# Kernel tuning notes

Measured on AMD Instinct MI355X. Metric: run time of the kernel, lower is better.

The kernel has to match this reference:

```python
import jax, jax.numpy as jnp
import numpy as np

COST_CLASS = 1.0
COST_BBOX = 5.0
COST_GIOU = 2.0
BS, NQ, NC, M = 16, 1000, 92, 1024


def box_cxcywh_to_xyxy(x):
    xc, yc, w, h = jnp.split(x, 4, axis=-1)
    return jnp.concatenate([xc - 0.5 * w, yc - 0.5 * h, xc + 0.5 * w, yc + 0.5 * h], axis=-1)


def generalized_box_iou(a, b):
    # a: [N,4] xyxy, b: [M,4] xyxy -> [N,M]
    area_a = (a[:, 2] - a[:, 0]) * (a[:, 3] - a[:, 1])
    area_b = (b[:, 2] - b[:, 0]) * (b[:, 3] - b[:, 1])
    lt = jnp.maximum(a[:, None, :2], b[None, :, :2])  # [N,M,2]
    rb = jnp.minimum(a[:, None, 2:], b[None, :, 2:])
    wh = jnp.clip(rb - lt, 0.0)
    inter = wh[..., 0] * wh[..., 1]
    union = area_a[:, None] + area_b[None, :] - inter
    iou = inter / union
    lt_e = jnp.minimum(a[:, None, :2], b[None, :, :2])
    rb_e = jnp.maximum(a[:, None, 2:], b[None, :, 2:])
    wh_e = jnp.clip(rb_e - lt_e, 0.0)
    area_e = wh_e[..., 0] * wh_e[..., 1]
    return iou - (area_e - union) / area_e


def setup_inputs() -> dict:
    key = jax.random.key(0)
    k1, k2, k3, k4 = jax.random.split(key, 4)
    return {
        'pred_logits': jax.random.normal(k1, (BS, NQ, NC), dtype=jnp.float32),
        'pred_boxes': jax.random.uniform(k2, (BS, NQ, 4), dtype=jnp.float32),
        'tgt_boxes': jax.random.uniform(k3, (M, 4), dtype=jnp.float32),
        'tgt_labels': jax.random.randint(k4, (M,), 0, NC),
    }


def reference(pred_logits, pred_boxes, tgt_boxes, tgt_labels):
    bs, nq, nc = pred_logits.shape
    out_prob = jax.nn.softmax(pred_logits.reshape(bs * nq, nc), axis=-1)
    out_bbox = pred_boxes.reshape(bs * nq, 4)
    tgt_ids = jnp.clip(tgt_labels, 0, nc - 1)
    # classification cost: -prob of target class, gathered per target -> [N, M]
    cost_class = -out_prob[:, tgt_ids]
    # L1 cdist on cxcywh boxes -> [N, M]
    cost_bbox = jnp.abs(out_bbox[:, None, :] - tgt_bbox_b(tgt_boxes)[None, :, :]).sum(-1)
    cost_giou = -generalized_box_iou(box_cxcywh_to_xyxy(out_bbox), box_cxcywh_to_xyxy(tgt_boxes))
    C = COST_BBOX * cost_bbox + COST_CLASS * cost_class + COST_GIOU * cost_giou
    return C.reshape(bs, nq, -1)


def tgt_bbox_b(tgt_boxes):
    return tgt_boxes
```

## Files before the change

kernel.cpp:

```cpp
#include <hip/hip_runtime.h>
#include <math.h>


#define NROWS 16000
#define NC 92
#define M_TGT 1024
#define TPB 256
#define ROWS 8
#define KPT 4

typedef float f32x4 __attribute__((ext_vector_type(4)));

__global__ __launch_bounds__(TPB, 6) void hungarian_cost_kernel(
    const float* __restrict__ logits,
    const float* __restrict__ pboxes,
    const float* __restrict__ tboxes,
    const int*   __restrict__ tlabels,
    float* __restrict__ out)
{
    const int n0 = blockIdx.x * ROWS;
    const int t = threadIdx.x;
    const int lane = t & 63;
    const int wid  = t >> 6;

    __shared__ float negp[ROWS][NC];

    #pragma unroll
    for (int j = 0; j < 2; ++j) {
        const int r = wid * 2 + j;
        const float* lg = logits + (size_t)(n0 + r) * NC;
        const float x0 = lg[lane];
        const bool  hi = (lane < NC - 64);
        const float x1 = hi ? lg[64 + lane] : -INFINITY;
        float mx = fmaxf(x0, x1);
        #pragma unroll
        for (int off = 32; off >= 1; off >>= 1)
            mx = fmaxf(mx, __shfl_xor(mx, off));
        const float e0 = __expf(x0 - mx);
        const float e1 = hi ? __expf(x1 - mx) : 0.0f;
        float s = e0 + e1;
        #pragma unroll
        for (int off = 32; off >= 1; off >>= 1)
            s += __shfl_xor(s, off);
        const float rs = __builtin_amdgcn_rcpf(s);
        negp[r][lane] = fmaf(-e0, rs, 2.0f);
        if (hi) negp[r][64 + lane] = fmaf(-e1, rs, 2.0f);
    }

    float tcx[KPT], tcy[KPT], twd[KPT], tht[KPT];
    float bx0[KPT], by0[KPT], bx1[KPT], by1[KPT], areab[KPT];
    const int4 lb4 = reinterpret_cast<const int4*>(tlabels)[t];
    int lbl[KPT] = {lb4.x, lb4.y, lb4.z, lb4.w};
    #pragma unroll
    for (int k = 0; k < KPT; ++k) {
        const float4 tb = reinterpret_cast<const float4*>(tboxes)[4 * t + k];
        tcx[k] = tb.x; tcy[k] = tb.y; twd[k] = tb.z; tht[k] = tb.w;
        bx0[k] = fmaf(-0.5f, tb.z, tb.x);  by0[k] = fmaf(-0.5f, tb.w, tb.y);
        bx1[k] = fmaf( 0.5f, tb.z, tb.x);  by1[k] = fmaf( 0.5f, tb.w, tb.y);
        areab[k] = tb.z * tb.w;
        lbl[k] = (lbl[k] < 0) ? 0 : (lbl[k] > NC - 1 ? NC - 1 : lbl[k]);
    }
    __syncthreads();

    float cls[KPT];
    #pragma unroll
    for (int k = 0; k < KPT; ++k) cls[k] = negp[0][lbl[k]];
    float4 pb = reinterpret_cast<const float4*>(pboxes)[n0];

    #pragma unroll
    for (int r = 0; r < ROWS; ++r) {
        float clsN[KPT];
        float4 pbN;
        if (r + 1 < ROWS) {
            #pragma unroll
            for (int k = 0; k < KPT; ++k) clsN[k] = negp[r + 1][lbl[k]];
            pbN = reinterpret_cast<const float4*>(pboxes)[n0 + r + 1];
        }

        const float ax0 = fmaf(-0.5f, pb.z, pb.x);
        const float ay0 = fmaf(-0.5f, pb.w, pb.y);
        const float ax1 = fmaf( 0.5f, pb.z, pb.x);
        const float ay1 = fmaf( 0.5f, pb.w, pb.y);
        const float area_a = pb.z * pb.w;

        float tmp[KPT];
        #pragma unroll
        for (int k = 0; k < KPT; ++k) {
            const float cb = fabsf(pb.x - tcx[k]) + fabsf(pb.y - tcy[k])
                           + fabsf(pb.z - twd[k]) + fabsf(pb.w - tht[k]);
            const float iwu = fminf(ax1, bx1[k]) - fmaxf(ax0, bx0[k]);
            const float ihu = fminf(ay1, by1[k]) - fmaxf(ay0, by0[k]);
            const float inter = fmaxf(iwu, 0.0f) * fmaxf(ihu, 0.0f);
            const float uni = area_a + areab[k] - inter;
            const float ew = pb.z + twd[k] - iwu;
            const float eh = pb.w + tht[k] - ihu;
            const float ae = ew * eh;
            const float h = fmaf(inter, __builtin_amdgcn_rcpf(uni),
                                 uni * __builtin_amdgcn_rcpf(ae));
            tmp[k] = fmaf(5.0f, cb, cls[k]) - 2.0f * h;
        }
        float4 res = {tmp[0], tmp[1], tmp[2], tmp[3]};
        reinterpret_cast<float4*>(out + ((size_t)(n0 + r) << 10))[t] = res;

        #pragma unroll
        for (int k = 0; k < KPT; ++k) cls[k] = clsN[k];
        pb = pbN;
    }
}

extern "C" void kernel_launch(void* const* d_in, const int* in_sizes, int n_in,
                              void* d_out, int out_size, void* d_ws, size_t ws_size,
                              hipStream_t stream) {
    const float* logits  = (const float*)d_in[0];
    const float* pboxes  = (const float*)d_in[1];
    const float* tboxes  = (const float*)d_in[2];
    const int*   tlabels = (const int*)d_in[3];
    float* out = (float*)d_out;

    hungarian_cost_kernel<<<NROWS / ROWS, TPB, 0, stream>>>(
        logits, pboxes, tboxes, tlabels, out);
}
```

Measured before the change: 24.34 us.

## Use one target per thread with 1024-thread blocks and nontemporal scalar stores

```diff
diff --git a/kernel.cpp b/kernel.cpp
--- a/kernel.cpp
+++ b/kernel.cpp
@@ -5,13 +5,10 @@
 #define NROWS 16000
 #define NC 92
 #define M_TGT 1024
-#define TPB 256
-#define ROWS 8
-#define KPT 4
+#define TPB 1024
+#define ROWS 32
 
-typedef float f32x4 __attribute__((ext_vector_type(4)));
-
-__global__ __launch_bounds__(TPB, 6) void hungarian_cost_kernel(
+__global__ __launch_bounds__(TPB, 2) void hungarian_cost_kernel(
     const float* __restrict__ logits,
     const float* __restrict__ pboxes,
     const float* __restrict__ tboxes,
@@ -47,33 +44,24 @@
         if (hi) negp[r][64 + lane] = fmaf(-e1, rs, 2.0f);
     }
 
-    float tcx[KPT], tcy[KPT], twd[KPT], tht[KPT];
-    float bx0[KPT], by0[KPT], bx1[KPT], by1[KPT], areab[KPT];
-    const int4 lb4 = reinterpret_cast<const int4*>(tlabels)[t];
-    int lbl[KPT] = {lb4.x, lb4.y, lb4.z, lb4.w};
-    #pragma unroll
-    for (int k = 0; k < KPT; ++k) {
-        const float4 tb = reinterpret_cast<const float4*>(tboxes)[4 * t + k];
-        tcx[k] = tb.x; tcy[k] = tb.y; twd[k] = tb.z; tht[k] = tb.w;
-        bx0[k] = fmaf(-0.5f, tb.z, tb.x);  by0[k] = fmaf(-0.5f, tb.w, tb.y);
-        bx1[k] = fmaf( 0.5f, tb.z, tb.x);  by1[k] = fmaf( 0.5f, tb.w, tb.y);
-        areab[k] = tb.z * tb.w;
-        lbl[k] = (lbl[k] < 0) ? 0 : (lbl[k] > NC - 1 ? NC - 1 : lbl[k]);
-    }
+    const float4 tb = reinterpret_cast<const float4*>(tboxes)[t];
+    const float tcx = tb.x, tcy = tb.y, twd = tb.z, tht = tb.w;
+    const float bx0 = fmaf(-0.5f, tb.z, tb.x), by0 = fmaf(-0.5f, tb.w, tb.y);
+    const float bx1 = fmaf( 0.5f, tb.z, tb.x), by1 = fmaf( 0.5f, tb.w, tb.y);
+    const float areab = tb.z * tb.w;
+    int lbl = tlabels[t];
+    lbl = (lbl < 0) ? 0 : (lbl > NC - 1 ? NC - 1 : lbl);
     __syncthreads();
 
-    float cls[KPT];
-    #pragma unroll
-    for (int k = 0; k < KPT; ++k) cls[k] = negp[0][lbl[k]];
+    float cls = negp[0][lbl];
     float4 pb = reinterpret_cast<const float4*>(pboxes)[n0];
 
-    #pragma unroll
+    #pragma unroll 4
     for (int r = 0; r < ROWS; ++r) {
-        float clsN[KPT];
+        float clsN;
         float4 pbN;
         if (r + 1 < ROWS) {
-            #pragma unroll
-            for (int k = 0; k < KPT; ++k) clsN[k] = negp[r + 1][lbl[k]];
+            clsN = negp[r + 1][lbl];
             pbN = reinterpret_cast<const float4*>(pboxes)[n0 + r + 1];
         }
 
@@ -83,27 +71,22 @@
         const float ay1 = fmaf( 0.5f, pb.w, pb.y);
         const float area_a = pb.z * pb.w;
 
-        float tmp[KPT];
-        #pragma unroll
-        for (int k = 0; k < KPT; ++k) {
-            const float cb = fabsf(pb.x - tcx[k]) + fabsf(pb.y - tcy[k])
-                           + fabsf(pb.z - twd[k]) + fabsf(pb.w - tht[k]);
-            const float iwu = fminf(ax1, bx1[k]) - fmaxf(ax0, bx0[k]);
-            const float ihu = fminf(ay1, by1[k]) - fmaxf(ay0, by0[k]);
-            const float inter = fmaxf(iwu, 0.0f) * fmaxf(ihu, 0.0f);
-            const float uni = area_a + areab[k] - inter;
-            const float ew = pb.z + twd[k] - iwu;
-            const float eh = pb.w + tht[k] - ihu;
-            const float ae = ew * eh;
-            const float h = fmaf(inter, __builtin_amdgcn_rcpf(uni),
-                                 uni * __builtin_amdgcn_rcpf(ae));
-            tmp[k] = fmaf(5.0f, cb, cls[k]) - 2.0f * h;
-        }
-        float4 res = {tmp[0], tmp[1], tmp[2], tmp[3]};
-        reinterpret_cast<float4*>(out + ((size_t)(n0 + r) << 10))[t] = res;
+        const float cb = fabsf(pb.x - tcx) + fabsf(pb.y - tcy)
+                       + fabsf(pb.z - twd) + fabsf(pb.w - tht);
+        const float iwu = fminf(ax1, bx1) - fmaxf(ax0, bx0);
+        const float ihu = fminf(ay1, by1) - fmaxf(ay0, by0);
+        const float inter = fmaxf(iwu, 0.0f) * fmaxf(ihu, 0.0f);
+        const float uni = area_a + areab - inter;
+        const float ew = pb.z + twd - iwu;
+        const float eh = pb.w + tht - ihu;
+        const float ae = ew * eh;
+        const float h = fmaf(inter, __builtin_amdgcn_rcpf(uni),
+                             uni * __builtin_amdgcn_rcpf(ae));
+        const float cost = fmaf(5.0f, cb, cls) - 2.0f * h;
 
-        #pragma unroll
-        for (int k = 0; k < KPT; ++k) cls[k] = clsN[k];
+        __builtin_nontemporal_store(cost, out + ((size_t)(n0 + r) << 10) + t);
+
+        cls = clsN;
         pb = pbN;
     }
 }
```

After: 24.47 us. Within noise of the previous version (+0.5%).
